# Optimization experiments

Hardware: AMD Instinct MI355X
Metric: run time of the kernel (lower is better)

The kernel has to match this reference:

```python
import jax, jax.numpy as jnp
import numpy as np

D_IN = 1024
D_H = 1024

def setup_inputs() -> dict:
    key = jax.random.key(0)
    ks = jax.random.split(key, 9)
    s = 1.0 / np.sqrt(D_IN)
    inp = {
        'x': jax.random.normal(ks[0], (4, 2048, D_IN), dtype=jnp.float32),
        'wq': jax.random.uniform(ks[1], (D_IN, D_H), jnp.float32, -s, s),
        'bq': jax.random.uniform(ks[2], (D_H,), jnp.float32, -s, s),
        'wk': jax.random.uniform(ks[3], (D_IN, D_H), jnp.float32, -s, s),
        'bk': jax.random.uniform(ks[4], (D_H,), jnp.float32, -s, s),
        'wv': jax.random.uniform(ks[5], (D_IN, D_H), jnp.float32, -s, s),
        'bv': jax.random.uniform(ks[6], (D_H,), jnp.float32, -s, s),
        'wo': jax.random.uniform(ks[7], (D_H, D_IN), jnp.float32, -s, s),
        'bo': jax.random.uniform(ks[8], (D_IN,), jnp.float32, -s, s),
    }
    return inp

def reference(x, wq, bq, wk, bk, wv, bv, wo, bo):
    # q,k,v: [b, s, d]
    q = x @ wq + bq
    k = x @ wk + bk
    v = x @ wv + bv
    scale = 1.0 / jnp.sqrt(jnp.asarray(D_H, x.dtype))
    attn = jnp.einsum('bqd,bkd->bqk', q, k) * scale  # [b, s, s]
    attn = jax.nn.softmax(attn, axis=-1)
    score = jnp.einsum('bqk,bkd->bqd', attn, v)
    out = score @ wo + bo
    return out
```

## Files before the change

### kernel.cpp

```cpp
#include <hip/hip_runtime.h>


typedef unsigned short u16;
typedef short bf16x8 __attribute__((ext_vector_type(8)));
typedef float f32x4 __attribute__((ext_vector_type(4)));

#define SEQ 2048
#define DIM 1024

__device__ __forceinline__ u16 f2bf(float f) {
    unsigned u = __builtin_bit_cast(unsigned, f);
    u += 0x7fffu + ((u >> 16) & 1u);
    return (u16)(u >> 16);
}

__device__ __forceinline__ void async16(void* lds, const void* gmem) {
    __builtin_amdgcn_global_load_lds(
        (const __attribute__((address_space(1))) void*)gmem,
        (__attribute__((address_space(3))) void*)lds, 16, 0, 0);
}

__global__ __launch_bounds__(256) void cast_x_kernel(
    const float* __restrict__ x, u16* __restrict__ xb,
    const float* __restrict__ bq, const float* __restrict__ bk,
    const float* __restrict__ bv, float* __restrict__ bqkv,
    float* __restrict__ l)
{
    const int b = blockIdx.x;
    if (b < 8192) {
        const int idx = b * 256 + threadIdx.x;
        float4 v = ((const float4*)x)[idx];
        ushort4 o;
        o.x = f2bf(v.x); o.y = f2bf(v.y); o.z = f2bf(v.z); o.w = f2bf(v.w);
        ((ushort4*)xb)[idx] = o;
    } else {
        const int i = (b - 8192) * 256 + threadIdx.x;
        if (i < 3072)
            bqkv[i] = (i < 1024) ? bq[i] : (i < 2048) ? bk[i - 1024] : bv[i - 2048];
        else if (i < 3072 + 8192)
            l[i - 3072] = 0.f;
    }
}

__global__ __launch_bounds__(256) void transpose_cast_all(
    const float* __restrict__ W0, const float* __restrict__ W1,
    const float* __restrict__ W2, const float* __restrict__ W3,
    u16* __restrict__ Tqkv, u16* __restrict__ To)
{
    __shared__ float tile[32][33];
    const int z = blockIdx.z;
    const float* W = (z == 0) ? W0 : (z == 1) ? W1 : (z == 2) ? W2 : W3;
    u16* T = (z < 3) ? (Tqkv + (size_t)z * 1048576) : To;

    const int bx = blockIdx.x * 32, by = blockIdx.y * 32;
    const int tx = threadIdx.x, ty = threadIdx.y;
    #pragma unroll
    for (int r = 0; r < 4; ++r)
        tile[ty + r * 8][tx] = W[(size_t)(by + ty + r * 8) * DIM + bx + tx];
    __syncthreads();
    #pragma unroll
    for (int r = 0; r < 4; ++r) {
        const float v = tile[tx][ty + r * 8];
        T[(size_t)(bx + ty + r * 8) * DIM + by + tx] = f2bf(v);
    }
}

#define EPI_QKV    0
#define EPI_ELOGIT 1
#define EPI_PV     2
#define EPI_OUT    4

template<int EPI, int K, int LDA, int LDB, int LDC>
__global__ __launch_bounds__(128, 2) void gemm2w(
    const u16* __restrict__ A, const u16* __restrict__ Bt,
    const float* __restrict__ bias, u16* __restrict__ C,
    u16* __restrict__ C2, float* __restrict__ Cf, float* __restrict__ lsum,
    float scale, long sA, long sB, long sC)
{
    __shared__ u16 sAm[128 * 32];
    __shared__ u16 sBm[128 * 32];

    const int z = blockIdx.z;
    A  += (size_t)z * sA;
    Bt += (size_t)z * sB;

    const int t  = threadIdx.x;
    const int m0 = blockIdx.y * 128, n0 = blockIdx.x * 128;
    const int wv = t >> 6, lane = t & 63;
    const int wm = wv * 64;
    const int lrow = lane & 15, quad = lane >> 4;
    const int sw = quad ^ ((lrow >> 1) & 3);

    f32x4 acc[4][8];
    #pragma unroll
    for (int i = 0; i < 4; ++i)
        #pragma unroll
        for (int j = 0; j < 8; ++j)
            acc[i][j] = (f32x4){0.f, 0.f, 0.f, 0.f};

    #pragma unroll 1
    for (int k0 = 0; k0 < K; k0 += 32) {
        #pragma unroll
        for (int p = 0; p < 4; ++p) {
            const int slot = p * 128 + t;
            const int row  = slot >> 2;
            const int c8   = (slot & 3) ^ ((row >> 1) & 3);
            async16(&sAm[slot * 8], &A[(size_t)(m0 + row) * LDA + k0 + c8 * 8]);
        }
        #pragma unroll
        for (int p = 0; p < 4; ++p) {
            const int slot = p * 128 + t;
            const int row  = slot >> 2;
            const int c8   = (slot & 3) ^ ((row >> 1) & 3);
            async16(&sBm[slot * 8], &Bt[(size_t)(n0 + row) * LDB + k0 + c8 * 8]);
        }
        __syncthreads();

        bf16x8 af[4], bf[8];
        #pragma unroll
        for (int i = 0; i < 4; ++i)
            af[i] = *(const bf16x8*)&sAm[((wm + i * 16 + lrow) * 4 + sw) * 8];
        #pragma unroll
        for (int j = 0; j < 8; ++j)
            bf[j] = *(const bf16x8*)&sBm[((j * 16 + lrow) * 4 + sw) * 8];
        #pragma unroll
        for (int i = 0; i < 4; ++i)
            #pragma unroll
            for (int j = 0; j < 8; ++j)
                acc[i][j] = __builtin_amdgcn_mfma_f32_16x16x32_bf16(
                    af[i], bf[j], acc[i][j], 0, 0, 0);
        __syncthreads();
    }

    if (EPI != EPI_OUT) C += (size_t)z * sC;

    #pragma unroll
    for (int i = 0; i < 4; ++i) {
        const int row = m0 + wm + i * 16 + quad * 4;
        if (EPI == EPI_QKV) {
            const int reg = (n0 >> 10);
            #pragma unroll
            for (int j = 0; j < 8; ++j) {
                const int col = n0 + j * 16 + lrow;
                const float b = bias[col];
                const f32x4 a = acc[i][j];
                if (reg < 2) {
                    const int c = col & 1023;
                    #pragma unroll
                    for (int r = 0; r < 4; ++r)
                        C[(size_t)reg * 8388608 + (size_t)(row + r) * 1024 + c]
                            = f2bf(a[r] + b);
                } else {
                    const int d = col & 1023;
                    const int bb = row >> 11, s0 = row & 2047;
                    ushort4 o;
                    o.x = f2bf(a[0] + b); o.y = f2bf(a[1] + b);
                    o.z = f2bf(a[2] + b); o.w = f2bf(a[3] + b);
                    *(ushort4*)&C2[(size_t)bb * (DIM * SEQ) + (size_t)d * SEQ + s0] = o;
                }
            }
        } else if (EPI == EPI_ELOGIT) {
            float rs[4] = {0.f, 0.f, 0.f, 0.f};
            #pragma unroll
            for (int j = 0; j < 8; ++j) {
                const int col = n0 + j * 16 + lrow;
                const f32x4 a = acc[i][j];
                #pragma unroll
                for (int r = 0; r < 4; ++r) {
                    const float e = __expf(a[r] * scale);
                    C[(size_t)(row + r) * LDC + col] = f2bf(e);
                    rs[r] += e;
                }
            }
            #pragma unroll
            for (int r = 0; r < 4; ++r) {
                float s = rs[r];
                s += __shfl_xor(s, 1, 64);
                s += __shfl_xor(s, 2, 64);
                s += __shfl_xor(s, 4, 64);
                s += __shfl_xor(s, 8, 64);
                if (lrow == 0)
                    atomicAdd(&lsum[(size_t)z * 2048 + row + r], s);
            }
        } else if (EPI == EPI_PV) {
            float linv[4];
            #pragma unroll
            for (int r = 0; r < 4; ++r)
                linv[r] = 1.0f / lsum[(size_t)z * 2048 + row + r];
            #pragma unroll
            for (int j = 0; j < 8; ++j) {
                const int col = n0 + j * 16 + lrow;
                const f32x4 a = acc[i][j];
                #pragma unroll
                for (int r = 0; r < 4; ++r)
                    C[(size_t)(row + r) * LDC + col] = f2bf(a[r] * linv[r]);
            }
        } else {
            #pragma unroll
            for (int j = 0; j < 8; ++j) {
                const int col = n0 + j * 16 + lrow;
                const float b = bias[col];
                const f32x4 a = acc[i][j];
                #pragma unroll
                for (int r = 0; r < 4; ++r)
                    Cf[(size_t)(row + r) * LDC + col] = a[r] + b;
            }
        }
    }
}

extern "C" void kernel_launch(void* const* d_in, const int* in_sizes, int n_in,
                              void* d_out, int out_size, void* d_ws, size_t ws_size,
                              hipStream_t stream)
{
    const float* x  = (const float*)d_in[0];
    const float* wq = (const float*)d_in[1];
    const float* bq = (const float*)d_in[2];
    const float* wk = (const float*)d_in[3];
    const float* bk = (const float*)d_in[4];
    const float* wv = (const float*)d_in[5];
    const float* bv = (const float*)d_in[6];
    const float* wo = (const float*)d_in[7];
    const float* bo = (const float*)d_in[8];
    float* out = (float*)d_out;

    u16* w16   = (u16*)d_ws;
    u16* xb    = w16;
    u16* q     = w16 + 8388608;
    u16* k_    = w16 + 16777216;
    u16* vT    = w16 + 25165824;
    u16* E     = w16 + 33554432;
    u16* wqkvT = w16 + 50331648;
    u16* woT   = w16 + 53477376;
    float* bqkv = (float*)(w16 + 54525952);
    float* l    = (float*)(w16 + 54532096);
    u16* sc    = w16;

    cast_x_kernel<<<8236, dim3(256), 0, stream>>>(x, xb, bq, bk, bv, bqkv, l);
    transpose_cast_all<<<dim3(32, 32, 4), dim3(32, 8), 0, stream>>>(
        wq, wk, wv, wo, wqkvT, woT);

    gemm2w<EPI_QKV, 1024, 1024, 1024, 1024>
        <<<dim3(24, 64, 1), dim3(128), 0, stream>>>(
            xb, wqkvT, bqkv, q, vT, nullptr, nullptr, 1.f, 0, 0, 0);

    gemm2w<EPI_ELOGIT, 1024, 1024, 1024, 2048>
        <<<dim3(16, 16, 4), dim3(128), 0, stream>>>(
            q, k_, nullptr, E, nullptr, nullptr, l, 0.03125f,
            2097152, 2097152, 4194304);

    gemm2w<EPI_PV, 2048, 2048, 2048, 1024>
        <<<dim3(8, 16, 4), dim3(128), 0, stream>>>(
            E, vT, nullptr, sc, nullptr, nullptr, l, 1.0f,
            4194304, 2097152, 2097152);

    gemm2w<EPI_OUT, 1024, 1024, 1024, 1024>
        <<<dim3(8, 64, 1), dim3(128), 0, stream>>>(
            sc, woT, bo, nullptr, nullptr, out, nullptr, 1.f, 0, 0, 0);
}
```

Measured before the change: 320.3 us.

## Fold Wo into V per batch and double-buffer LDS in GEMM main loop

```diff
diff --git a/kernel.cpp b/kernel.cpp
--- a/kernel.cpp
+++ b/kernel.cpp
@@ -65,20 +65,20 @@
     }
 }
 
-#define EPI_QKV    0
-#define EPI_ELOGIT 1
-#define EPI_PV     2
-#define EPI_OUT    4
+#define EPI_BF16BIAS 0
+#define EPI_BF16     1
+#define EPI_ELOGIT   2
+#define EPI_PVOUT    3
 
 template<int EPI, int K, int LDA, int LDB, int LDC>
 __global__ __launch_bounds__(128, 2) void gemm2w(
     const u16* __restrict__ A, const u16* __restrict__ Bt,
     const float* __restrict__ bias, u16* __restrict__ C,
-    u16* __restrict__ C2, float* __restrict__ Cf, float* __restrict__ lsum,
+    float* __restrict__ Cf, float* __restrict__ lsum,
     float scale, long sA, long sB, long sC)
 {
-    __shared__ u16 sAm[128 * 32];
-    __shared__ u16 sBm[128 * 32];
+    __shared__ u16 sA0[128 * 32], sB0[128 * 32];
+    __shared__ u16 sA1[128 * 32], sB1[128 * 32];
 
     const int z = blockIdx.z;
     A  += (size_t)z * sA;
@@ -98,66 +98,78 @@
         for (int j = 0; j < 8; ++j)
             acc[i][j] = (f32x4){0.f, 0.f, 0.f, 0.f};
 
-    #pragma unroll 1
-    for (int k0 = 0; k0 < K; k0 += 32) {
+    auto stage = [&](u16* dA, u16* dB, int k0) {
         #pragma unroll
         for (int p = 0; p < 4; ++p) {
             const int slot = p * 128 + t;
             const int row  = slot >> 2;
             const int c8   = (slot & 3) ^ ((row >> 1) & 3);
-            async16(&sAm[slot * 8], &A[(size_t)(m0 + row) * LDA + k0 + c8 * 8]);
+            async16(&dA[slot * 8], &A[(size_t)(m0 + row) * LDA + k0 + c8 * 8]);
         }
         #pragma unroll
         for (int p = 0; p < 4; ++p) {
             const int slot = p * 128 + t;
             const int row  = slot >> 2;
             const int c8   = (slot & 3) ^ ((row >> 1) & 3);
-            async16(&sBm[slot * 8], &Bt[(size_t)(n0 + row) * LDB + k0 + c8 * 8]);
+            async16(&dB[slot * 8], &Bt[(size_t)(n0 + row) * LDB + k0 + c8 * 8]);
         }
-        __syncthreads();
-
+    };
+    auto compute = [&](const u16* bA, const u16* bB) {
         bf16x8 af[4], bf[8];
         #pragma unroll
         for (int i = 0; i < 4; ++i)
-            af[i] = *(const bf16x8*)&sAm[((wm + i * 16 + lrow) * 4 + sw) * 8];
+            af[i] = *(const bf16x8*)&bA[((wm + i * 16 + lrow) * 4 + sw) * 8];
         #pragma unroll
         for (int j = 0; j < 8; ++j)
-            bf[j] = *(const bf16x8*)&sBm[((j * 16 + lrow) * 4 + sw) * 8];
+            bf[j] = *(const bf16x8*)&bB[((j * 16 + lrow) * 4 + sw) * 8];
         #pragma unroll
         for (int i = 0; i < 4; ++i)
             #pragma unroll
             for (int j = 0; j < 8; ++j)
                 acc[i][j] = __builtin_amdgcn_mfma_f32_16x16x32_bf16(
                     af[i], bf[j], acc[i][j], 0, 0, 0);
+    };
+
+    stage(sA0, sB0, 0);
+    __syncthreads();
+    #pragma unroll 1
+    for (int k0 = 0; k0 + 64 < K; k0 += 64) {
+        stage(sA1, sB1, k0 + 32);
+        compute(sA0, sB0);
         __syncthreads();
-    }
-
-    if (EPI != EPI_OUT) C += (size_t)z * sC;
+        stage(sA0, sB0, k0 + 64);
+        compute(sA1, sB1);
+        __syncthreads();
+    }
+    stage(sA1, sB1, K - 32);
+    compute(sA0, sB0);
+    __syncthreads();
+    compute(sA1, sB1);
+
+    if (EPI == EPI_PVOUT) Cf += (size_t)z * sC;
+    else                  C  += (size_t)z * sC;
 
     #pragma unroll
     for (int i = 0; i < 4; ++i) {
         const int row = m0 + wm + i * 16 + quad * 4;
-        if (EPI == EPI_QKV) {
-            const int reg = (n0 >> 10);
+        if (EPI == EPI_BF16BIAS) {
             #pragma unroll
             for (int j = 0; j < 8; ++j) {
                 const int col = n0 + j * 16 + lrow;
                 const float b = bias[col];
                 const f32x4 a = acc[i][j];
-                if (reg < 2) {
-                    const int c = col & 1023;
-                    #pragma unroll
-                    for (int r = 0; r < 4; ++r)
-                        C[(size_t)reg * 8388608 + (size_t)(row + r) * 1024 + c]
-                            = f2bf(a[r] + b);
-                } else {
-                    const int d = col & 1023;
-                    const int bb = row >> 11, s0 = row & 2047;
-                    ushort4 o;
-                    o.x = f2bf(a[0] + b); o.y = f2bf(a[1] + b);
-                    o.z = f2bf(a[2] + b); o.w = f2bf(a[3] + b);
-                    *(ushort4*)&C2[(size_t)bb * (DIM * SEQ) + (size_t)d * SEQ + s0] = o;
-                }
+                #pragma unroll
+                for (int r = 0; r < 4; ++r)
+                    C[(size_t)(row + r) * LDC + col] = f2bf(a[r] + b);
+            }
+        } else if (EPI == EPI_BF16) {
+            #pragma unroll
+            for (int j = 0; j < 8; ++j) {
+                const int col = n0 + j * 16 + lrow;
+                const f32x4 a = acc[i][j];
+                #pragma unroll
+                for (int r = 0; r < 4; ++r)
+                    C[(size_t)(row + r) * LDC + col] = f2bf(a[r]);
             }
         } else if (EPI == EPI_ELOGIT) {
             float rs[4] = {0.f, 0.f, 0.f, 0.f};
@@ -182,7 +194,7 @@
                 if (lrow == 0)
                     atomicAdd(&lsum[(size_t)z * 2048 + row + r], s);
             }
-        } else if (EPI == EPI_PV) {
+        } else {
             float linv[4];
             #pragma unroll
             for (int r = 0; r < 4; ++r)
@@ -190,20 +202,11 @@
             #pragma unroll
             for (int j = 0; j < 8; ++j) {
                 const int col = n0 + j * 16 + lrow;
+                const float b = bias[col];
                 const f32x4 a = acc[i][j];
                 #pragma unroll
                 for (int r = 0; r < 4; ++r)
-                    C[(size_t)(row + r) * LDC + col] = f2bf(a[r] * linv[r]);
-            }
-        } else {
-            #pragma unroll
-            for (int j = 0; j < 8; ++j) {
-                const int col = n0 + j * 16 + lrow;
-                const float b = bias[col];
-                const f32x4 a = acc[i][j];
-                #pragma unroll
-                for (int r = 0; r < 4; ++r)
-                    Cf[(size_t)(row + r) * LDC + col] = a[r] + b;
+                    Cf[(size_t)(row + r) * LDC + col] = a[r] * linv[r] + b;
             }
         }
     }
@@ -226,35 +229,38 @@
 
     u16* w16   = (u16*)d_ws;
     u16* xb    = w16;
-    u16* q     = w16 + 8388608;
-    u16* k_    = w16 + 16777216;
-    u16* vT    = w16 + 25165824;
+    u16* qkv   = w16 + 8388608;
     u16* E     = w16 + 33554432;
     u16* wqkvT = w16 + 50331648;
     u16* woT   = w16 + 53477376;
     float* bqkv = (float*)(w16 + 54525952);
     float* l    = (float*)(w16 + 54532096);
-    u16* sc    = w16;
+    u16* VWoT  = w16;
+
+    const u16* q_ = qkv;
+    const u16* k_ = qkv + 1024;
+    const u16* v_ = qkv + 2048;
 
     cast_x_kernel<<<8236, dim3(256), 0, stream>>>(x, xb, bq, bk, bv, bqkv, l);
     transpose_cast_all<<<dim3(32, 32, 4), dim3(32, 8), 0, stream>>>(
         wq, wk, wv, wo, wqkvT, woT);
 
-    gemm2w<EPI_QKV, 1024, 1024, 1024, 1024>
+    gemm2w<EPI_BF16BIAS, 1024, 1024, 1024, 3072>
         <<<dim3(24, 64, 1), dim3(128), 0, stream>>>(
-            xb, wqkvT, bqkv, q, vT, nullptr, nullptr, 1.f, 0, 0, 0);
-
-    gemm2w<EPI_ELOGIT, 1024, 1024, 1024, 2048>
+            xb, wqkvT, bqkv, qkv, nullptr, nullptr, 1.f, 0, 0, 0);
+
+    gemm2w<EPI_ELOGIT, 1024, 3072, 3072, 2048>
         <<<dim3(16, 16, 4), dim3(128), 0, stream>>>(
-            q, k_, nullptr, E, nullptr, nullptr, l, 0.03125f,
-            2097152, 2097152, 4194304);
-
-    gemm2w<EPI_PV, 2048, 2048, 2048, 1024>
+            q_, k_, nullptr, E, nullptr, l, 0.03125f,
+            6291456, 6291456, 4194304);
+
+    gemm2w<EPI_BF16, 1024, 1024, 3072, 2048>
+        <<<dim3(16, 8, 4), dim3(128), 0, stream>>>(
+            woT, v_, nullptr, VWoT, nullptr, nullptr, 1.f,
+            0, 6291456, 2097152);
+
+    gemm2w<EPI_PVOUT, 2048, 2048, 2048, 1024>
         <<<dim3(8, 16, 4), dim3(128), 0, stream>>>(
-            E, vT, nullptr, sc, nullptr, nullptr, l, 1.0f,
+            E, VWoT, bo, nullptr, out, l, 1.f,
             4194304, 2097152, 2097152);
-
-    gemm2w<EPI_OUT, 1024, 1024, 1024, 1024>
-        <<<dim3(8, 64, 1), dim3(128), 0, stream>>>(
-            sc, woT, bo, nullptr, nullptr, out, nullptr, 1.f, 0, 0, 0);
-}
+}
```

New measurement: 304.3 us. 1.05x faster.
